# Kernel tuning notes

Hardware: AMD Instinct MI355X
Metric: run time of the kernel (lower is better)

Reference implementation:

```python
import jax, jax.numpy as jnp
import numpy as np

N_COND, K, D = 16, 512, 256
B, H, W = 32, 64, 64


def setup_inputs() -> dict:
    key = jax.random.key(0)
    k1, k2, k3 = jax.random.split(key, 3)
    z_e_x = jax.random.normal(k1, (B, D, H, W), dtype=jnp.float32)
    C = jax.random.randint(k2, (B,), 0, N_COND, dtype=jnp.int64)
    bound = 1.0 / (K * N_COND)
    weight = jax.random.uniform(k3, (N_COND, K, D), dtype=jnp.float32,
                                minval=-bound, maxval=bound)
    return {"z_e_x": z_e_x, "C": C, "weight": weight}


def reference(z_e_x, C, weight):
    b, d, h, w = z_e_x.shape
    # [B, H, W, D] -> [B, N, D] with N = H*W
    z = jnp.transpose(z_e_x, (0, 2, 3, 1)).reshape(b, h * w, d)
    cb = weight[C]  # per-sample codebook [B, K, D] (batched gather replaces python loop)
    # squared euclidean distances: ||z||^2 - 2 z.e + ||e||^2  -> [B, N, K]
    dist = (jnp.sum(z * z, axis=-1, keepdims=True)
            - 2.0 * jnp.einsum('bnd,bkd->bnk', z, cb)
            + jnp.sum(cb * cb, axis=-1)[:, None, :])
    idx = jnp.argmin(dist, axis=-1)  # [B, N]
    quant = jnp.take_along_axis(cb, idx[..., None], axis=1)  # [B, N, D]
    # straight-through output (vq_st): forward = quantized
    z_q = z + jax.lax.stop_gradient(quant - z)
    # z_q_x_bar: plain gather from (non-detached) codebook
    z_q_bar = quant
    z_q_x = jnp.transpose(z_q.reshape(b, h, w, d), (0, 3, 1, 2))
    z_q_x_bar = jnp.transpose(z_q_bar.reshape(b, h, w, d), (0, 3, 1, 2))
    return z_q_x, z_q_x_bar
```

## Files before the change

kernel.cpp:

```cpp
#include <hip/hip_runtime.h>
#include <cfloat>

#define NB    32
#define ND    256
#define NK    512
#define NCOND 16
#define NHW   4096
#define PXT   64
#define MARGIN 1.3e-4f
#define QCAP  16

typedef __attribute__((ext_vector_type(8))) short bf16x8;
typedef __attribute__((ext_vector_type(4))) float f32x4;

__device__ __forceinline__ int loadC(const int* __restrict__ C, int b) {
  int orodd = 0;
#pragma unroll
  for (int i = 1; i < 32; i += 2) orodd |= C[i];
  return (orodd == 0) ? C[2 * b] : C[b];
}

__device__ __forceinline__ unsigned short rne_bf16(float x) {
  unsigned u = __float_as_uint(x);
  u += 0x7fffu + ((u >> 16) & 1u);
  return (unsigned short)(u >> 16);
}

__device__ __forceinline__ void gl2lds16(const void* g, void* l) {
  __builtin_amdgcn_global_load_lds(
      (const __attribute__((address_space(1))) void*)g,
      (__attribute__((address_space(3))) void*)l, 16, 0, 0);
}

__device__ float np_score_g(const float* __restrict__ z, size_t zoff,
                            const float* __restrict__ er, float S) {
  float P0 = 0.f, P1 = 0.f, P2 = 0.f, P3 = 0.f;
  for (int ch = 0; ch < 16; ++ch) {
    const float* eb = er + ch * 16;
    float4 e0 = *(const float4*)(eb + 0);
    float4 e1 = *(const float4*)(eb + 4);
    float4 e2 = *(const float4*)(eb + 8);
    float4 e3 = *(const float4*)(eb + 12);
    float zb[16];
#pragma unroll
    for (int q = 0; q < 16; ++q)
      zb[q] = z[zoff + (size_t)(ch * 16 + q) * NHW];
    P0 = __fadd_rn(P0, __fmul_rn(zb[12], e3.x));
    P0 = __fadd_rn(P0, __fmul_rn(zb[8],  e2.x));
    P0 = __fadd_rn(P0, __fmul_rn(zb[4],  e1.x));
    P0 = __fadd_rn(P0, __fmul_rn(zb[0],  e0.x));
    P1 = __fadd_rn(P1, __fmul_rn(zb[13], e3.y));
    P1 = __fadd_rn(P1, __fmul_rn(zb[9],  e2.y));
    P1 = __fadd_rn(P1, __fmul_rn(zb[5],  e1.y));
    P1 = __fadd_rn(P1, __fmul_rn(zb[1],  e0.y));
    P2 = __fadd_rn(P2, __fmul_rn(zb[14], e3.z));
    P2 = __fadd_rn(P2, __fmul_rn(zb[10], e2.z));
    P2 = __fadd_rn(P2, __fmul_rn(zb[6],  e1.z));
    P2 = __fadd_rn(P2, __fmul_rn(zb[2],  e0.z));
    P3 = __fadd_rn(P3, __fmul_rn(zb[15], e3.w));
    P3 = __fadd_rn(P3, __fmul_rn(zb[11], e2.w));
    P3 = __fadd_rn(P3, __fmul_rn(zb[7],  e1.w));
    P3 = __fadd_rn(P3, __fmul_rn(zb[3],  e0.w));
  }
  float G = __fadd_rn(__fadd_rn(P0, P1), __fadd_rn(P2, P3));
  return __fadd_rn(S, __fmul_rn(-2.0f, G));
}

__global__ __launch_bounds__(256) void k_split(
    const float* __restrict__ w, unsigned short* __restrict__ whi) {
  int i = (blockIdx.x * 256 + threadIdx.x) * 4;
  float4 v = *(const float4*)&w[i];
  int ci = i >> 17, rem = i & 131071;
  int code = rem >> 8, d = rem & 255;
  int dst = (ci << 17) + ((d >> 5) << 14) + (code << 5) + (d & 31);
  ushort4 h;
  h.x = rne_bf16(v.x); h.y = rne_bf16(v.y);
  h.z = rne_bf16(v.z); h.w = rne_bf16(v.w);
  *(ushort4*)&whi[dst] = h;
}

template <int PRE>
__global__ __launch_bounds__(512, 4) void k_vq(
    const float* __restrict__ z, const int* __restrict__ Cc,
    const float* __restrict__ w, const unsigned short* __restrict__ whi,
    float* __restrict__ out) {
  __shared__ __align__(16) unsigned short EsH[NK * 32];
  __shared__ float Ssh[PXT];
  __shared__ float Wmin[8][32];
  __shared__ float Thr[PXT];
  __shared__ int   qcnt[PXT], KB[PXT];
  __shared__ int   qk[PXT][QCAP];

  int orig = blockIdx.x;
  int blk  = (orig & 7) * 256 + (orig >> 3);
  int b    = blk >> 6;
  int n0   = (blk & 63) * PXT;
  int c    = loadC(Cc, b);
  int t    = threadIdx.x;
  int lane = t & 63;
  int wv   = t >> 6;
  int mw   = wv >> 2;
  int nw   = wv & 3;

  if (t < PXT) qcnt[t] = 0;

  const size_t zab = (size_t)b * ND * NHW;
  const size_t cbu = (size_t)c * (NK * ND);
  const int ar_n = n0 + mw * 32 + (lane & 15);
  const int koff = (lane >> 4) * 8;

  f32x4 acc0[8], acc1[8];
#pragma unroll
  for (int nt = 0; nt < 8; ++nt) {
    acc0[nt] = (f32x4){0.f, 0.f, 0.f, 0.f};
    acc1[nt] = (f32x4){0.f, 0.f, 0.f, 0.f};
  }

  float zf0[8], zf1[8];
  const float* zA = z + zab + ar_n;

#pragma unroll 1
  for (int ks = 0; ks < 8; ++ks) {
    __syncthreads();
    if constexpr (PRE) {
#pragma unroll
      for (int p = 0; p < 4; ++p) {
        int code = p * 128 + wv * 16 + (lane >> 2);
        int ql   = (lane & 3) ^ ((code >> 1) & 3);
        const unsigned short* src = whi + cbu + ks * (NK * 32) + code * 32 + ql * 8;
        gl2lds16(src, &EsH[(p * 512 + wv * 64) * 8]);
      }
    } else {
#pragma unroll
      for (int p = 0; p < 4; ++p) {
        int code = p * 128 + (t >> 2);
        int ql   = t & 3;
        const float* sf = w + ((size_t)c * NK + code) * ND + ks * 32 + ql * 8;
        float4 f0 = *(const float4*)sf;
        float4 f1 = *(const float4*)(sf + 4);
        float xs[8] = {f0.x, f0.y, f0.z, f0.w, f1.x, f1.y, f1.z, f1.w};
        bf16x8 h;
#pragma unroll
        for (int q = 0; q < 8; ++q) h[q] = (short)rne_bf16(xs[q]);
        int phys = ql ^ ((code >> 1) & 3);
        *(bf16x8*)&EsH[code * 32 + phys * 8] = h;
      }
    }
#pragma unroll
    for (int j = 0; j < 8; ++j) {
      size_t doff = (size_t)(ks * 32 + koff + j) * NHW;
      zf0[j] = zA[doff];
      zf1[j] = zA[doff + 16];
    }
    __syncthreads();

    bf16x8 ah0, al0, ah1, al1;
#pragma unroll
    for (int j = 0; j < 8; ++j) {
      unsigned u0 = __float_as_uint(zf0[j]) & 0xffff0000u;
      ah0[j] = (short)(u0 >> 16);
      al0[j] = (short)rne_bf16(zf0[j] - __uint_as_float(u0));
      unsigned u1 = __float_as_uint(zf1[j]) & 0xffff0000u;
      ah1[j] = (short)(u1 >> 16);
      al1[j] = (short)rne_bf16(zf1[j] - __uint_as_float(u1));
    }
#pragma unroll
    for (int nt = 0; nt < 8; ++nt) {
      int code = nw * 128 + nt * 16 + (lane & 15);
      int phys = (lane >> 4) ^ ((code >> 1) & 3);
      bf16x8 bh = *(const bf16x8*)&EsH[code * 32 + phys * 8];
      acc0[nt] = __builtin_amdgcn_mfma_f32_16x16x32_bf16(ah0, bh, acc0[nt], 0, 0, 0);
      acc0[nt] = __builtin_amdgcn_mfma_f32_16x16x32_bf16(al0, bh, acc0[nt], 0, 0, 0);
      acc1[nt] = __builtin_amdgcn_mfma_f32_16x16x32_bf16(ah1, bh, acc1[nt], 0, 0, 0);
      acc1[nt] = __builtin_amdgcn_mfma_f32_16x16x32_bf16(al1, bh, acc1[nt], 0, 0, 0);
    }
  }

  {
    int spx = t >> 3, sj = t & 7;
    size_t sb = zab + n0 + spx;
    float r0 = 0.f, r1 = 0.f;
#pragma unroll
    for (int i = 0; i < 16; ++i) {
      float v0 = z[sb + (size_t)(8 * i + sj) * NHW];
      float v1 = z[sb + (size_t)(128 + 8 * i + sj) * NHW];
      r0 = __fadd_rn(r0, __fmul_rn(v0, v0));
      r1 = __fadd_rn(r1, __fmul_rn(v1, v1));
    }
#pragma unroll
    for (int off = 1; off < 8; off <<= 1) {
      r0 = __fadd_rn(r0, __shfl_xor(r0, off));
      r1 = __fadd_rn(r1, __shfl_xor(r1, off));
    }
    if (sj == 0) Ssh[spx] = __fadd_rn(r0, r1);
  }
  __syncthreads();

  float pmin0[4], pmin1[4], S40[4], S41[4];
#pragma unroll
  for (int r = 0; r < 4; ++r) {
    int pr = mw * 32 + (lane >> 4) * 4 + r;
    S40[r] = Ssh[pr];
    S41[r] = Ssh[pr + 16];
    pmin0[r] = FLT_MAX; pmin1[r] = FLT_MAX;
  }
#pragma unroll
  for (int nt = 0; nt < 8; ++nt)
#pragma unroll
    for (int r = 0; r < 4; ++r) {
      float X0 = __fadd_rn(S40[r], __fmul_rn(-2.0f, acc0[nt][r]));
      float X1 = __fadd_rn(S41[r], __fmul_rn(-2.0f, acc1[nt][r]));
      acc0[nt][r] = X0; acc1[nt][r] = X1;
      pmin0[r] = fminf(pmin0[r], X0);
      pmin1[r] = fminf(pmin1[r], X1);
    }
#pragma unroll
  for (int r = 0; r < 4; ++r)
#pragma unroll
    for (int off = 1; off < 16; off <<= 1) {
      pmin0[r] = fminf(pmin0[r], __shfl_xor(pmin0[r], off));
      pmin1[r] = fminf(pmin1[r], __shfl_xor(pmin1[r], off));
    }
  if ((lane & 15) == 0) {
#pragma unroll
    for (int r = 0; r < 4; ++r) {
      Wmin[wv][(lane >> 4) * 4 + r]      = pmin0[r];
      Wmin[wv][16 + (lane >> 4) * 4 + r] = pmin1[r];
    }
  }
  __syncthreads();
  if (t < PXT) {
    int m2 = (t >> 5) * 4, i = t & 31;
    Thr[t] = fminf(fminf(Wmin[m2][i], Wmin[m2 + 1][i]),
                   fminf(Wmin[m2 + 2][i], Wmin[m2 + 3][i])) + MARGIN;
  }
  __syncthreads();

#pragma unroll
  for (int r = 0; r < 4; ++r) {
    int px0 = mw * 32 + (lane >> 4) * 4 + r;
    float th0 = Thr[px0], th1 = Thr[px0 + 16];
#pragma unroll
    for (int nt = 0; nt < 8; ++nt) {
      int kcode = nw * 128 + nt * 16 + (lane & 15);
      if (acc0[nt][r] <= th0) {
        int slot = atomicAdd(&qcnt[px0], 1);
        if (slot < QCAP) qk[px0][slot] = kcode;
      }
      if (acc1[nt][r] <= th1) {
        int slot = atomicAdd(&qcnt[px0 + 16], 1);
        if (slot < QCAP) qk[px0 + 16][slot] = kcode;
      }
    }
  }
  __syncthreads();

  {
    int px  = wv * 8 + (lane >> 3);
    int cnt = qcnt[px]; cnt = cnt < QCAP ? cnt : QCAP;
    float S = Ssh[px];
    size_t zoff = zab + n0 + px;
    float bv = FLT_MAX; int bk = 0x7fffffff;
#pragma unroll
    for (int m = 0; m < 2; ++m) {
      int slot = (lane & 7) + 8 * m;
      if (__any(slot < cnt)) {
        if (slot < cnt) {
          int k = qk[px][slot];
          float v = np_score_g(z, zoff, w + ((size_t)c * NK + k) * ND, S);
          if (v < bv || (v == bv && k < bk)) { bv = v; bk = k; }
        }
      }
    }
#pragma unroll
    for (int off = 1; off < 8; off <<= 1) {
      float ov = __shfl_xor(bv, off);
      int   ok = __shfl_xor(bk, off);
      if (ov < bv || (ov == bv && ok < bk)) { bv = ov; bk = ok; }
    }
    if ((lane & 7) == 0) KB[px] = bk;
  }
  __syncthreads();

  {
    int px = t & 63, dg = t >> 6;
    int kidx = KB[px];
    const float* er = w + ((size_t)c * NK + kidx) * ND;
    const size_t OUT2 = (size_t)NB * ND * NHW;
    size_t base = zab + n0 + px;
#pragma unroll
    for (int j = 0; j < 32; ++j) {
      int d = dg * 32 + j;
      float q  = er[d];
      float zv = z[base + (size_t)d * NHW];
      out[base + (size_t)d * NHW]        = __fadd_rn(zv, __fsub_rn(q, zv));
      out[base + (size_t)d * NHW + OUT2] = q;
    }
  }
}

extern "C" void kernel_launch(void* const* d_in, const int* in_sizes, int n_in,
                              void* d_out, int out_size, void* d_ws, size_t ws_size,
                              hipStream_t stream) {
  const float* z = (const float*)d_in[0];
  const int*   C = (const int*)d_in[1];
  const float* w = (const float*)d_in[2];
  float* out = (float*)d_out;

  const size_t NWEL = (size_t)NCOND * NK * ND;
  unsigned short* whi = (unsigned short*)d_ws;
  bool pre = ws_size >= NWEL * sizeof(unsigned short);

  if (pre) {
    k_split<<<(int)(NWEL / 1024), 256, 0, stream>>>(w, whi);
    k_vq<1><<<NB * (NHW / PXT), 512, 0, stream>>>(z, C, w, whi, out);
  } else {
    k_vq<0><<<NB * (NHW / PXT), 512, 0, stream>>>(z, C, w, whi, out);
  }
}
```

Baseline: 243.6 us.

## Stage split z tile in LDS and stream codebook fragments directly from global

The whole 64-pixel z tile is converted once into bf16 hi/lo halves and stored in swizzled LDS. The MFMA loop then reads A fragments from LDS and B fragments (codebook bf16) straight from global/L2 instead of staging the codebook through LDS each k-step. This removes the per-step barriers and async LDS copies. The cost is LDS use of 64 KB per block, which may cut occupancy, and uncoalesced, latency-exposed global loads for the codebook inside the MFMA loop.

```diff
diff --git a/kernel.cpp b/kernel.cpp
--- a/kernel.cpp
+++ b/kernel.cpp
@@ -24,12 +24,6 @@
   unsigned u = __float_as_uint(x);
   u += 0x7fffu + ((u >> 16) & 1u);
   return (unsigned short)(u >> 16);
-}
-
-__device__ __forceinline__ void gl2lds16(const void* g, void* l) {
-  __builtin_amdgcn_global_load_lds(
-      (const __attribute__((address_space(1))) void*)g,
-      (__attribute__((address_space(3))) void*)l, 16, 0, 0);
 }
 
 __device__ float np_score_g(const float* __restrict__ z, size_t zoff,
@@ -79,12 +73,17 @@
   *(ushort4*)&whi[dst] = h;
 }
 
+__device__ __forceinline__ int zofs(int px, int chunk) {
+  return px * 256 + ((chunk ^ (px & 7)) * 8);
+}
+
 template <int PRE>
 __global__ __launch_bounds__(512, 4) void k_vq(
     const float* __restrict__ z, const int* __restrict__ Cc,
     const float* __restrict__ w, const unsigned short* __restrict__ whi,
     float* __restrict__ out) {
-  __shared__ __align__(16) unsigned short EsH[NK * 32];
+  __shared__ __align__(16) unsigned short Zh[PXT * ND];
+  __shared__ __align__(16) unsigned short Zl[PXT * ND];
   __shared__ float Ssh[PXT];
   __shared__ float Wmin[8][32];
   __shared__ float Thr[PXT];
@@ -106,73 +105,25 @@
 
   const size_t zab = (size_t)b * ND * NHW;
   const size_t cbu = (size_t)c * (NK * ND);
-  const int ar_n = n0 + mw * 32 + (lane & 15);
+  const int ar0  = mw * 32 + (lane & 15);
   const int koff = (lane >> 4) * 8;
 
-  f32x4 acc0[8], acc1[8];
-#pragma unroll
-  for (int nt = 0; nt < 8; ++nt) {
-    acc0[nt] = (f32x4){0.f, 0.f, 0.f, 0.f};
-    acc1[nt] = (f32x4){0.f, 0.f, 0.f, 0.f};
-  }
-
-  float zf0[8], zf1[8];
-  const float* zA = z + zab + ar_n;
-
-#pragma unroll 1
-  for (int ks = 0; ks < 8; ++ks) {
-    __syncthreads();
-    if constexpr (PRE) {
-#pragma unroll
-      for (int p = 0; p < 4; ++p) {
-        int code = p * 128 + wv * 16 + (lane >> 2);
-        int ql   = (lane & 3) ^ ((code >> 1) & 3);
-        const unsigned short* src = whi + cbu + ks * (NK * 32) + code * 32 + ql * 8;
-        gl2lds16(src, &EsH[(p * 512 + wv * 64) * 8]);
-      }
-    } else {
-#pragma unroll
-      for (int p = 0; p < 4; ++p) {
-        int code = p * 128 + (t >> 2);
-        int ql   = t & 3;
-        const float* sf = w + ((size_t)c * NK + code) * ND + ks * 32 + ql * 8;
-        float4 f0 = *(const float4*)sf;
-        float4 f1 = *(const float4*)(sf + 4);
-        float xs[8] = {f0.x, f0.y, f0.z, f0.w, f1.x, f1.y, f1.z, f1.w};
-        bf16x8 h;
-#pragma unroll
-        for (int q = 0; q < 8; ++q) h[q] = (short)rne_bf16(xs[q]);
-        int phys = ql ^ ((code >> 1) & 3);
-        *(bf16x8*)&EsH[code * 32 + phys * 8] = h;
-      }
-    }
-#pragma unroll
-    for (int j = 0; j < 8; ++j) {
-      size_t doff = (size_t)(ks * 32 + koff + j) * NHW;
-      zf0[j] = zA[doff];
-      zf1[j] = zA[doff + 16];
-    }
-    __syncthreads();
-
-    bf16x8 ah0, al0, ah1, al1;
-#pragma unroll
-    for (int j = 0; j < 8; ++j) {
-      unsigned u0 = __float_as_uint(zf0[j]) & 0xffff0000u;
-      ah0[j] = (short)(u0 >> 16);
-      al0[j] = (short)rne_bf16(zf0[j] - __uint_as_float(u0));
-      unsigned u1 = __float_as_uint(zf1[j]) & 0xffff0000u;
-      ah1[j] = (short)(u1 >> 16);
-      al1[j] = (short)rne_bf16(zf1[j] - __uint_as_float(u1));
-    }
-#pragma unroll
-    for (int nt = 0; nt < 8; ++nt) {
-      int code = nw * 128 + nt * 16 + (lane & 15);
-      int phys = (lane >> 4) ^ ((code >> 1) & 3);
-      bf16x8 bh = *(const bf16x8*)&EsH[code * 32 + phys * 8];
-      acc0[nt] = __builtin_amdgcn_mfma_f32_16x16x32_bf16(ah0, bh, acc0[nt], 0, 0, 0);
-      acc0[nt] = __builtin_amdgcn_mfma_f32_16x16x32_bf16(al0, bh, acc0[nt], 0, 0, 0);
-      acc1[nt] = __builtin_amdgcn_mfma_f32_16x16x32_bf16(ah1, bh, acc1[nt], 0, 0, 0);
-      acc1[nt] = __builtin_amdgcn_mfma_f32_16x16x32_bf16(al1, bh, acc1[nt], 0, 0, 0);
+  {
+    int px = t & 63, dg = t >> 6;
+    const float* zp = z + zab + n0 + px;
+#pragma unroll
+    for (int cc4 = 0; cc4 < 4; ++cc4) {
+      int chunk = dg * 4 + cc4;
+      bf16x8 h, l;
+#pragma unroll
+      for (int j = 0; j < 8; ++j) {
+        float v = zp[(size_t)(chunk * 8 + j) * NHW];
+        unsigned u = __float_as_uint(v) & 0xffff0000u;
+        h[j] = (short)(u >> 16);
+        l[j] = (short)rne_bf16(v - __uint_as_float(u));
+      }
+      *(bf16x8*)&Zh[zofs(px, chunk)] = h;
+      *(bf16x8*)&Zl[zofs(px, chunk)] = l;
     }
   }
 
@@ -195,6 +146,41 @@
     if (sj == 0) Ssh[spx] = __fadd_rn(r0, r1);
   }
   __syncthreads();
+
+  f32x4 acc0[8], acc1[8];
+#pragma unroll
+  for (int nt = 0; nt < 8; ++nt) {
+    acc0[nt] = (f32x4){0.f, 0.f, 0.f, 0.f};
+    acc1[nt] = (f32x4){0.f, 0.f, 0.f, 0.f};
+  }
+
+#pragma unroll 1
+  for (int ks = 0; ks < 8; ++ks) {
+    int chunkA = ks * 4 + (lane >> 4);
+    bf16x8 ah0 = *(const bf16x8*)&Zh[zofs(ar0,      chunkA)];
+    bf16x8 al0 = *(const bf16x8*)&Zl[zofs(ar0,      chunkA)];
+    bf16x8 ah1 = *(const bf16x8*)&Zh[zofs(ar0 + 16, chunkA)];
+    bf16x8 al1 = *(const bf16x8*)&Zl[zofs(ar0 + 16, chunkA)];
+#pragma unroll
+    for (int nt = 0; nt < 8; ++nt) {
+      int code = nw * 128 + nt * 16 + (lane & 15);
+      bf16x8 bh;
+      if constexpr (PRE) {
+        bh = *(const bf16x8*)(whi + cbu + ks * (NK * 32) + code * 32 + koff);
+      } else {
+        const float* sf = w + ((size_t)c * NK + code) * ND + ks * 32 + koff;
+        float4 f0 = *(const float4*)sf;
+        float4 f1 = *(const float4*)(sf + 4);
+        float xs[8] = {f0.x, f0.y, f0.z, f0.w, f1.x, f1.y, f1.z, f1.w};
+#pragma unroll
+        for (int q = 0; q < 8; ++q) bh[q] = (short)rne_bf16(xs[q]);
+      }
+      acc0[nt] = __builtin_amdgcn_mfma_f32_16x16x32_bf16(ah0, bh, acc0[nt], 0, 0, 0);
+      acc0[nt] = __builtin_amdgcn_mfma_f32_16x16x32_bf16(al0, bh, acc0[nt], 0, 0, 0);
+      acc1[nt] = __builtin_amdgcn_mfma_f32_16x16x32_bf16(ah1, bh, acc1[nt], 0, 0, 0);
+      acc1[nt] = __builtin_amdgcn_mfma_f32_16x16x32_bf16(al1, bh, acc1[nt], 0, 0, 0);
+    }
+  }
 
   float pmin0[4], pmin1[4], S40[4], S41[4];
 #pragma unroll
```

After: 233.2 us. -4.3%, faster.
